# Kernel optimization log

Measured on AMD Instinct MI355X. Metric: run time of the kernel, lower is better.

Reference implementation:

```python
import jax, jax.numpy as jnp
import numpy as np
import math

B, S, H, NH = 1, 2048, 1024, 16  # batch, seq, hidden, heads


def setup_inputs() -> dict:
    key = jax.random.key(0)
    ks = jax.random.split(key, 12)
    inp = {
        "query": jax.random.normal(ks[0], (B, S, H), dtype=jnp.float32),
        "key": jax.random.normal(ks[1], (B, S, H), dtype=jnp.float32),
        "value": jax.random.normal(ks[2], (B, S, H), dtype=jnp.float32),
        "attention_mask": jax.random.randint(ks[3], (1, 1, S, S), 0, 2, dtype=jnp.int32),
        # torch nn.Linear params: y = x @ W.T + b, W init ~ U(-1/sqrt(H), 1/sqrt(H))
        "Wq": jax.random.uniform(ks[4], (H, H), jnp.float32, -1, 1) / math.sqrt(H),
        "bq": jax.random.uniform(ks[5], (H,), jnp.float32, -1, 1) / math.sqrt(H),
        "Wk": jax.random.uniform(ks[6], (H, H), jnp.float32, -1, 1) / math.sqrt(H),
        "bk": jax.random.uniform(ks[7], (H,), jnp.float32, -1, 1) / math.sqrt(H),
        "Wv": jax.random.uniform(ks[8], (H, H), jnp.float32, -1, 1) / math.sqrt(H),
        "bv": jax.random.uniform(ks[9], (H,), jnp.float32, -1, 1) / math.sqrt(H),
        "Wo": jax.random.uniform(ks[10], (H, H), jnp.float32, -1, 1) / math.sqrt(H),
        "bo": jax.random.uniform(ks[11], (H,), jnp.float32, -1, 1) / math.sqrt(H),
        "head": NH,
        "hidden_size": H,
    }
    return inp


def reference(query, key, value, attention_mask, Wq, bq, Wk, bk, Wv, bv, Wo, bo, head, hidden_size):
    b, s, _ = query.shape
    d_k = hidden_size // head

    def proj(x, W, bias):
        # [b, s, hidden] -> [b, head, s, d_k]
        y = x @ W.T + bias
        return y.reshape(b, s, head, d_k).transpose(0, 2, 1, 3)

    q = proj(query, Wq, bq)
    k = proj(key, Wk, bk)
    v = proj(value, Wv, bv)

    # naive full score matrix, as in the source (scale by sqrt(d_k) = last dim of q)
    scores = jnp.einsum("bhqd,bhkd->bhqk", q, k) / math.sqrt(d_k)
    # faithful quirk: masked positions are set to 0 (not -inf) before softmax
    scores = jnp.where(attention_mask == 0, jnp.zeros((), scores.dtype), scores)
    attn = jax.nn.softmax(scores, axis=-1)

    out = jnp.einsum("bhqk,bhkd->bhqd", attn, v)  # [b, head, s, d_k]
    out = out.transpose(0, 2, 1, 3).reshape(b, s, head * d_k)
    return out @ Wo.T + bo
```

## Files before the change

### kernel.cpp

```cpp
#include <hip/hip_runtime.h>
#include <hip/hip_bf16.h>


#define S_LEN 2048
#define HID   1024
#define NHEAD 16
#define DK    64

typedef unsigned short u16;
typedef __attribute__((ext_vector_type(8))) short bf16x8;
typedef __attribute__((ext_vector_type(4))) short bf16x4;
typedef __attribute__((ext_vector_type(4))) float f32x4;

__device__ __forceinline__ void load16_lds(const void* g, void* l) {
  __builtin_amdgcn_global_load_lds(
      (const __attribute__((address_space(1))) void*)g,
      (__attribute__((address_space(3))) void*)l, 16, 0, 0);
}

__device__ __forceinline__ short bfbits(float x) {
  __hip_bfloat16 h = __float2bfloat16(x);
  return *(short*)&h;
}
__device__ __forceinline__ bf16x8 cvt8(float4 a, float4 b) {
  bf16x8 r;
  r[0] = bfbits(a.x); r[1] = bfbits(a.y); r[2] = bfbits(a.z); r[3] = bfbits(a.w);
  r[4] = bfbits(b.x); r[5] = bfbits(b.y); r[6] = bfbits(b.z); r[7] = bfbits(b.w);
  return r;
}
__device__ __forceinline__ float bf2f(u16 u) {
  unsigned v = (unsigned)u << 16;
  return *(float*)&v;
}

__global__ __launch_bounds__(256) void cvtW_kernel(
    const float* __restrict__ wq, const float* __restrict__ wk,
    const float* __restrict__ wv, const float* __restrict__ wo,
    u16* __restrict__ Wbf) {
  const int y = blockIdx.y;
  const float* src = y == 0 ? wq : (y == 1 ? wk : (y == 2 ? wv : wo));
  size_t i = ((size_t)blockIdx.x * 256 + threadIdx.x) * 8;
  float4 a = *(const float4*)(src + i);
  float4 b = *(const float4*)(src + i + 4);
  *(bf16x8*)(Wbf + (size_t)y * (HID * HID) + i) = cvt8(a, b);
}

__global__ void pack_mask_kernel(const int* __restrict__ mask,
                                 unsigned int* __restrict__ bits) {
  int w = blockIdx.x * blockDim.x + threadIdx.x;
  const int4* p = (const int4*)(mask + (size_t)w * 32);
  unsigned word = 0;
#pragma unroll
  for (int i = 0; i < 8; ++i) {
    int4 v = p[i];
    word |= (unsigned)(v.x != 0) << (i * 4 + 0);
    word |= (unsigned)(v.y != 0) << (i * 4 + 1);
    word |= (unsigned)(v.z != 0) << (i * 4 + 2);
    word |= (unsigned)(v.w != 0) << (i * 4 + 3);
  }
  bits[w] = word;
}

__global__ __launch_bounds__(256) void gemm_bt(
    const void* A0, const void* A1, const void* A2, int a_fp32,
    const u16* __restrict__ Wbase,
    const float* b0, const float* b1, const float* b2,
    void* C0, void* C1, void* C2,
    int store_fp32, int transpose_z2, int qscale_z0) {
  constexpr int Mm = 2048, Nn = 1024, Kk = 1024;
  const int z = blockIdx.z;
  const void* A    = z == 0 ? A0 : (z == 1 ? A1 : A2);
  const u16*  W    = Wbase + (size_t)z * (Nn * Kk);
  const float* bias = z == 0 ? b0 : (z == 1 ? b1 : b2);
  void*       C    = z == 0 ? C0 : (z == 1 ? C1 : C2);
  const int transpose = (z == 2) ? transpose_z2 : 0;
  const float oscale = (z == 0 && qscale_z0) ? 0.125f : 1.0f;

  const int tid  = threadIdx.x;
  const int lane = tid & 63, wave = tid >> 6;
  const int q4 = lane >> 4, c16 = lane & 15;
  const int mBase = blockIdx.y * 128, nBase = blockIdx.x * 128;
  const int wm = (wave >> 1) * 64, wn = (wave & 1) * 64;

  __shared__ __align__(16) u16 As[128 * 32];
  __shared__ __align__(16) u16 Bs[128 * 32];

  f32x4 acc[4][4] = {};

  const int srow = lane >> 2;
  const int skk  = (lane & 3) * 8;

  const u16*   Ab = (const u16*)A;
  const float* Af = (const float*)A;

  for (int k0 = 0; k0 < Kk; k0 += 32) {
    float4 apre[4];
    if (a_fp32) {
#pragma unroll
      for (int i = 0; i < 2; ++i) {
        const float* s = Af + (size_t)(mBase + (wave * 2 + i) * 16 + srow) * Kk +
                         k0 + skk;
        apre[2 * i]     = *(const float4*)s;
        apre[2 * i + 1] = *(const float4*)(s + 4);
      }
    }
    __syncthreads();
    if (a_fp32) {
#pragma unroll
      for (int i = 0; i < 2; ++i) {
        int ch = wave * 2 + i;
        *(bf16x8*)&As[ch * 512 + srow * 32 + skk] =
            cvt8(apre[2 * i], apre[2 * i + 1]);
      }
    } else {
#pragma unroll
      for (int i = 0; i < 2; ++i) {
        int ch = wave * 2 + i;
        load16_lds(Ab + (size_t)(mBase + ch * 16 + srow) * Kk + k0 + skk,
                   &As[ch * 512]);
      }
    }
#pragma unroll
    for (int i = 0; i < 2; ++i) {
      int ch = wave * 2 + i;
      load16_lds(W + (size_t)(nBase + ch * 16 + srow) * Kk + k0 + skk,
                 &Bs[ch * 512]);
    }
    __syncthreads();

    bf16x8 af[4], bfr[4];
#pragma unroll
    for (int t = 0; t < 4; ++t) {
      af[t]  = *(const bf16x8*)&As[(wm + t * 16 + c16) * 32 + q4 * 8];
      bfr[t] = *(const bf16x8*)&Bs[(wn + t * 16 + c16) * 32 + q4 * 8];
    }
#pragma unroll
    for (int mt = 0; mt < 4; ++mt)
#pragma unroll
      for (int nt = 0; nt < 4; ++nt)
        acc[mt][nt] = __builtin_amdgcn_mfma_f32_16x16x32_bf16(
            af[mt], bfr[nt], acc[mt][nt], 0, 0, 0);
  }

#pragma unroll
  for (int nt = 0; nt < 4; ++nt) {
    int col = nBase + wn + nt * 16 + c16;
    float bv = bias[col];
#pragma unroll
    for (int mt = 0; mt < 4; ++mt) {
#pragma unroll
      for (int r = 0; r < 4; ++r) {
        int row = mBase + wm + mt * 16 + q4 * 4 + r;
        float v = (acc[mt][nt][r] + bv) * oscale;
        if (store_fp32)
          ((float*)C)[(size_t)row * Nn + col] = v;
        else if (transpose)
          ((__hip_bfloat16*)C)[(size_t)col * Mm + row] = __float2bfloat16(v);
        else
          ((__hip_bfloat16*)C)[(size_t)row * Nn + col] = __float2bfloat16(v);
      }
    }
  }
}

__global__ __launch_bounds__(256) void attn_kernel(
    const u16* __restrict__ Qb, const u16* __restrict__ Kb,
    const u16* __restrict__ Vt, const unsigned* __restrict__ mbits,
    u16* __restrict__ partO, float* __restrict__ partL) {
  const int qt = blockIdx.x;
  const int h  = blockIdx.y;
  const int zz = blockIdx.z;
  const int tid  = threadIdx.x;
  const int lane = tid & 63, wave = tid >> 6;
  const int q4 = lane >> 4, c16 = lane & 15;

  __shared__ __align__(16) u16 Ks[2][64 * 32];
  __shared__ __align__(16) u16 Vs[2][64 * 32];
  __shared__ __align__(16) u16 Ps[4][2 * 16 * 72];

  const int wq0 = qt * 128 + wave * 32;

  bf16x8 qf[2][2];
#pragma unroll
  for (int t = 0; t < 2; ++t)
#pragma unroll
    for (int kk = 0; kk < 2; ++kk)
      qf[t][kk] = *(const bf16x8*)(Qb + (size_t)(wq0 + t * 16 + c16) * HID +
                                   h * DK + kk * 32 + q4 * 8);

  f32x4 o[2][4] = {};
  float l_lane[2][4] = {};

  const int srow = lane >> 2;
  const int se8  = (lane & 3) * 8;
  const int kvbase = zz * (S_LEN / 2);

  for (int it = 0; it < S_LEN / 2 / 64; ++it) {
    const int kv0 = kvbase + it * 64;
    __syncthreads();
#pragma unroll
    for (int j = 0; j < 2; ++j) {
      int ch = wave * 2 + j;
      int half = ch >> 2, grp = ch & 3;
      load16_lds(Kb + (size_t)(kv0 + grp * 16 + srow) * HID + h * DK +
                     half * 32 + se8,
                 &Ks[half][grp * 512]);
      load16_lds(Vt + (size_t)(h * DK + grp * 16 + srow) * S_LEN + kv0 +
                     half * 32 + se8,
                 &Vs[half][grp * 512]);
    }
    __syncthreads();

    f32x4 sv[2][4];
#pragma unroll
    for (int nt = 0; nt < 4; ++nt) {
      bf16x8 kf0 = *(const bf16x8*)&Ks[0][(nt * 16 + c16) * 32 + q4 * 8];
      bf16x8 kf1 = *(const bf16x8*)&Ks[1][(nt * 16 + c16) * 32 + q4 * 8];
#pragma unroll
      for (int t = 0; t < 2; ++t) {
        f32x4 a = {};
        a = __builtin_amdgcn_mfma_f32_16x16x32_bf16(qf[t][0], kf0, a, 0, 0, 0);
        a = __builtin_amdgcn_mfma_f32_16x16x32_bf16(qf[t][1], kf1, a, 0, 0, 0);
        sv[t][nt] = a;
      }
    }

#pragma unroll
    for (int t = 0; t < 2; ++t)
#pragma unroll
      for (int r = 0; r < 4; ++r) {
        int row = wq0 + t * 16 + q4 * 4 + r;
        const unsigned* mrow = mbits + (size_t)row * 64 + (kv0 >> 5);
        unsigned w0 = mrow[0], w1 = mrow[1];
#pragma unroll
        for (int nt = 0; nt < 4; ++nt) {
          unsigned word = (nt < 2) ? w0 : w1;
          int bit = ((nt & 1) * 16) + c16;
          float s = ((word >> bit) & 1u) ? sv[t][nt][r] : 0.0f;
          float p = __expf(s);
          sv[t][nt][r] = p;
          l_lane[t][r] += p;
        }
      }

    u16* pw = &Ps[wave][0];
#pragma unroll
    for (int t = 0; t < 2; ++t)
#pragma unroll
      for (int r = 0; r < 4; ++r)
#pragma unroll
        for (int nt = 0; nt < 4; ++nt)
          ((__hip_bfloat16*)pw)[t * 1152 + (q4 * 4 + r) * 72 + nt * 16 + c16] =
              __float2bfloat16(sv[t][nt][r]);
    asm volatile("s_waitcnt lgkmcnt(0)" ::: "memory");

    bf16x8 vb[2][4];
#pragma unroll
    for (int kk = 0; kk < 2; ++kk)
#pragma unroll
      for (int nt = 0; nt < 4; ++nt)
        vb[kk][nt] = *(const bf16x8*)&Vs[kk][(nt * 16 + c16) * 32 + q4 * 8];
#pragma unroll
    for (int t = 0; t < 2; ++t)
#pragma unroll
      for (int kk = 0; kk < 2; ++kk) {
        bf16x8 pa = *(const bf16x8*)&pw[t * 1152 + c16 * 72 + kk * 32 + q4 * 8];
#pragma unroll
        for (int nt = 0; nt < 4; ++nt)
          o[t][nt] = __builtin_amdgcn_mfma_f32_16x16x32_bf16(pa, vb[kk][nt],
                                                             o[t][nt], 0, 0, 0);
      }
  }

#pragma unroll
  for (int t = 0; t < 2; ++t)
#pragma unroll
    for (int r = 0; r < 4; ++r) {
      float s = l_lane[t][r];
#pragma unroll
      for (int d = 1; d < 16; d <<= 1) s += __shfl_xor(s, d);
      l_lane[t][r] = s;
    }

#pragma unroll
  for (int t = 0; t < 2; ++t)
#pragma unroll
    for (int r = 0; r < 4; ++r) {
      int row = wq0 + t * 16 + q4 * 4 + r;
#pragma unroll
      for (int nt = 0; nt < 4; ++nt)
        ((__hip_bfloat16*)partO)[((size_t)zz * S_LEN + row) * HID + h * DK +
                                 nt * 16 + c16] = __float2bfloat16(o[t][nt][r]);
      if (c16 == 0)
        partL[((size_t)zz * NHEAD + h) * S_LEN + row] = l_lane[t][r];
    }
}

__global__ __launch_bounds__(256) void combine_kernel(
    const u16* __restrict__ partO, const float* __restrict__ partL,
    u16* __restrict__ ctx) {
  size_t idx = ((size_t)blockIdx.x * 256 + threadIdx.x) * 4;
  int row = (int)(idx >> 10);
  int col = (int)(idx & 1023);
  int h = col >> 6;
  float l = partL[(size_t)h * S_LEN + row] +
            partL[((size_t)NHEAD + h) * S_LEN + row];
  float inv = 1.0f / l;
  bf16x4 a = *(const bf16x4*)(partO + idx);
  bf16x4 b = *(const bf16x4*)(partO + (size_t)S_LEN * HID + idx);
  bf16x4 r;
#pragma unroll
  for (int j = 0; j < 4; ++j) {
    float v = (bf2f((u16)a[j]) + bf2f((u16)b[j])) * inv;
    r[j] = bfbits(v);
  }
  *(bf16x4*)(ctx + idx) = r;
}

extern "C" void kernel_launch(void* const* d_in, const int* in_sizes, int n_in,
                              void* d_out, int out_size, void* d_ws, size_t ws_size,
                              hipStream_t stream) {
  const float* q    = (const float*)d_in[0];
  const float* k    = (const float*)d_in[1];
  const float* v    = (const float*)d_in[2];
  const int*   mask = (const int*)d_in[3];
  const float* Wq = (const float*)d_in[4];
  const float* bq = (const float*)d_in[5];
  const float* Wk = (const float*)d_in[6];
  const float* bk = (const float*)d_in[7];
  const float* Wv = (const float*)d_in[8];
  const float* bv = (const float*)d_in[9];
  const float* Wo = (const float*)d_in[10];
  const float* bo = (const float*)d_in[11];

  const size_t M2 = (size_t)S_LEN * HID;
  const size_t need = (4 + 2 + 2 + 2 + 2) * M2 * 2 +
                      (size_t)S_LEN * 64 * 4 + 2 * NHEAD * S_LEN * 4;
  if (ws_size < need) return;

  u16* Wbf   = (u16*)d_ws;
  u16* partO = Wbf + 4 * (size_t)HID * HID / 2 * 2;
  u16* Qb    = partO + 2 * M2;
  u16* Kb    = Qb + M2;
  u16* Vt    = Kb + M2;
  unsigned* mbits = (unsigned*)(Vt + M2);
  float* partL = (float*)(mbits + (size_t)S_LEN * 64);
  u16* ctx = Qb;

  hipLaunchKernelGGL(cvtW_kernel, dim3(512, 4), dim3(256), 0, stream,
                     Wq, Wk, Wv, Wo, Wbf);

  hipLaunchKernelGGL(pack_mask_kernel, dim3((S_LEN * (S_LEN / 32)) / 256),
                     dim3(256), 0, stream, mask, mbits);

  hipLaunchKernelGGL(gemm_bt, dim3(HID / 128, S_LEN / 128, 3), dim3(256), 0,
                     stream, q, k, v, 1, Wbf, bq, bk, bv,
                     Qb, Kb, Vt, 0, 1, 1);

  hipLaunchKernelGGL(attn_kernel, dim3(S_LEN / 128, NHEAD, 2), dim3(256), 0,
                     stream, Qb, Kb, Vt, mbits, partO, partL);

  hipLaunchKernelGGL(combine_kernel, dim3((S_LEN * HID / 4) / 256), dim3(256),
                     0, stream, partO, partL, ctx);

  hipLaunchKernelGGL(gemm_bt, dim3(HID / 128, S_LEN / 128, 1), dim3(256), 0,
                     stream, ctx, ctx, ctx, 0, Wbf + 3 * (size_t)HID * HID,
                     bo, bo, bo, d_out, d_out, d_out, 1, 0, 0);
}
```

Before: 231.0 us.

## Double-buffer GEMM and attention LDS loads, template GEMM tile sizes

```diff
diff --git a/kernel.cpp b/kernel.cpp
--- a/kernel.cpp
+++ b/kernel.cpp
@@ -61,13 +61,20 @@
   bits[w] = word;
 }
 
+template <int BM, bool ABF>
 __global__ __launch_bounds__(256) void gemm_bt(
-    const void* A0, const void* A1, const void* A2, int a_fp32,
+    const void* A0, const void* A1, const void* A2,
     const u16* __restrict__ Wbase,
     const float* b0, const float* b1, const float* b2,
     void* C0, void* C1, void* C2,
     int store_fp32, int transpose_z2, int qscale_z0) {
-  constexpr int Mm = 2048, Nn = 1024, Kk = 1024;
+  constexpr int Mm = 2048, Nn = 1024, Kk = 1024, BK = 64;
+  constexpr int NIT = Kk / BK;
+  constexpr int MT = BM / 32;
+  constexpr int MTILES = Mm / BM;
+  constexpr int AG = BM / 16;
+  constexpr int AU = 2 * AG / 4;
+
   const int z = blockIdx.z;
   const void* A    = z == 0 ? A0 : (z == 1 ? A1 : A2);
   const u16*  W    = Wbase + (size_t)z * (Nn * Kk);
@@ -76,70 +83,100 @@
   const int transpose = (z == 2) ? transpose_z2 : 0;
   const float oscale = (z == 0 && qscale_z0) ? 0.125f : 1.0f;
 
-  const int tid  = threadIdx.x;
-  const int lane = tid & 63, wave = tid >> 6;
+  const int tid = threadIdx.x, lane = tid & 63, wave = tid >> 6;
   const int q4 = lane >> 4, c16 = lane & 15;
-  const int mBase = blockIdx.y * 128, nBase = blockIdx.x * 128;
-  const int wm = (wave >> 1) * 64, wn = (wave & 1) * 64;
-
-  __shared__ __align__(16) u16 As[128 * 32];
-  __shared__ __align__(16) u16 Bs[128 * 32];
-
-  f32x4 acc[4][4] = {};
+  const int bLin = blockIdx.x + blockIdx.y * gridDim.x;
+  const int mBase = (bLin & (MTILES - 1)) * BM;
+  const int nBase = (bLin / MTILES) * 128;
+  const int wm = (wave >> 1) * (BM / 2), wn = (wave & 1) * 64;
+
+  __shared__ __align__(16) u16 As[2][2][BM * 32];
+  __shared__ __align__(16) u16 Bs[2][2][128 * 32];
+
+  f32x4 acc[MT][4] = {};
 
   const int srow = lane >> 2;
-  const int skk  = (lane & 3) * 8;
+  const int se8  = (lane & 3) * 8;
 
   const u16*   Ab = (const u16*)A;
   const float* Af = (const float*)A;
 
-  for (int k0 = 0; k0 < Kk; k0 += 32) {
-    float4 apre[4];
-    if (a_fp32) {
-#pragma unroll
-      for (int i = 0; i < 2; ++i) {
-        const float* s = Af + (size_t)(mBase + (wave * 2 + i) * 16 + srow) * Kk +
-                         k0 + skk;
-        apre[2 * i]     = *(const float4*)s;
-        apre[2 * i + 1] = *(const float4*)(s + 4);
-      }
-    }
+  auto issueW = [&](int it, int buf) {
+#pragma unroll
+    for (int j = 0; j < 4; ++j) {
+      int i = wave * 4 + j;
+      int h = i >> 3, grp = i & 7;
+      load16_lds(W + (size_t)(nBase + grp * 16 + srow) * Kk + it * BK +
+                     h * 32 + se8,
+                 &Bs[buf][h][grp * 512]);
+    }
+  };
+  auto issueA = [&](int it, int buf) {
+#pragma unroll
+    for (int j = 0; j < AU; ++j) {
+      int i = wave * AU + j;
+      int h = i / AG, grp = i % AG;
+      load16_lds(Ab + (size_t)(mBase + grp * 16 + srow) * Kk + it * BK +
+                     h * 32 + se8,
+                 &As[buf][h][grp * 512]);
+    }
+  };
+  float4 ar[AU][2];
+  auto loadA = [&](int it) {
+#pragma unroll
+    for (int j = 0; j < AU; ++j) {
+      int i = wave * AU + j;
+      int h = i / AG, grp = i % AG;
+      const float* s = Af + (size_t)(mBase + grp * 16 + srow) * Kk + it * BK +
+                       h * 32 + se8;
+      ar[j][0] = *(const float4*)s;
+      ar[j][1] = *(const float4*)(s + 4);
+    }
+  };
+  auto storeA = [&](int buf) {
+#pragma unroll
+    for (int j = 0; j < AU; ++j) {
+      int i = wave * AU + j;
+      int h = i / AG, grp = i % AG;
+      *(bf16x8*)&As[buf][h][grp * 512 + srow * 32 + se8] =
+          cvt8(ar[j][0], ar[j][1]);
+    }
+  };
+
+  issueW(0, 0);
+  if (ABF) {
+    issueA(0, 0);
+  } else {
+    loadA(0);
+    storeA(0);
+  }
+  __syncthreads();
+
+  for (int it = 0; it < NIT; ++it) {
+    const int buf = it & 1, nbuf = buf ^ 1;
+    if (it + 1 < NIT) {
+      issueW(it + 1, nbuf);
+      if (ABF) issueA(it + 1, nbuf);
+      else     loadA(it + 1);
+    }
+#pragma unroll
+    for (int kk = 0; kk < 2; ++kk) {
+      bf16x8 af[MT], bfr[4];
+#pragma unroll
+      for (int t = 0; t < MT; ++t)
+        af[t] = *(const bf16x8*)&As[buf][kk][(wm + t * 16 + c16) * 32 + q4 * 8];
+#pragma unroll
+      for (int t = 0; t < 4; ++t)
+        bfr[t] = *(const bf16x8*)&Bs[buf][kk][(wn + t * 16 + c16) * 32 + q4 * 8];
+#pragma unroll
+      for (int mt = 0; mt < MT; ++mt)
+#pragma unroll
+        for (int nt = 0; nt < 4; ++nt)
+          acc[mt][nt] = __builtin_amdgcn_mfma_f32_16x16x32_bf16(
+              af[mt], bfr[nt], acc[mt][nt], 0, 0, 0);
+    }
+    if (!ABF && it + 1 < NIT) storeA(nbuf);
     __syncthreads();
-    if (a_fp32) {
-#pragma unroll
-      for (int i = 0; i < 2; ++i) {
-        int ch = wave * 2 + i;
-        *(bf16x8*)&As[ch * 512 + srow * 32 + skk] =
-            cvt8(apre[2 * i], apre[2 * i + 1]);
-      }
-    } else {
-#pragma unroll
-      for (int i = 0; i < 2; ++i) {
-        int ch = wave * 2 + i;
-        load16_lds(Ab + (size_t)(mBase + ch * 16 + srow) * Kk + k0 + skk,
-                   &As[ch * 512]);
-      }
-    }
-#pragma unroll
-    for (int i = 0; i < 2; ++i) {
-      int ch = wave * 2 + i;
-      load16_lds(W + (size_t)(nBase + ch * 16 + srow) * Kk + k0 + skk,
-                 &Bs[ch * 512]);
-    }
-    __syncthreads();
-
-    bf16x8 af[4], bfr[4];
-#pragma unroll
-    for (int t = 0; t < 4; ++t) {
-      af[t]  = *(const bf16x8*)&As[(wm + t * 16 + c16) * 32 + q4 * 8];
-      bfr[t] = *(const bf16x8*)&Bs[(wn + t * 16 + c16) * 32 + q4 * 8];
-    }
-#pragma unroll
-    for (int mt = 0; mt < 4; ++mt)
-#pragma unroll
-      for (int nt = 0; nt < 4; ++nt)
-        acc[mt][nt] = __builtin_amdgcn_mfma_f32_16x16x32_bf16(
-            af[mt], bfr[nt], acc[mt][nt], 0, 0, 0);
   }
 
 #pragma unroll
@@ -147,7 +184,7 @@
     int col = nBase + wn + nt * 16 + c16;
     float bv = bias[col];
 #pragma unroll
-    for (int mt = 0; mt < 4; ++mt) {
+    for (int mt = 0; mt < MT; ++mt) {
 #pragma unroll
       for (int r = 0; r < 4; ++r) {
         int row = mBase + wm + mt * 16 + q4 * 4 + r;
@@ -167,15 +204,13 @@
     const u16* __restrict__ Qb, const u16* __restrict__ Kb,
     const u16* __restrict__ Vt, const unsigned* __restrict__ mbits,
     u16* __restrict__ partO, float* __restrict__ partL) {
-  const int qt = blockIdx.x;
-  const int h  = blockIdx.y;
-  const int zz = blockIdx.z;
-  const int tid  = threadIdx.x;
-  const int lane = tid & 63, wave = tid >> 6;
+  constexpr int NITA = S_LEN / 2 / 64;
+  const int qt = blockIdx.x, h = blockIdx.y, zz = blockIdx.z;
+  const int tid = threadIdx.x, lane = tid & 63, wave = tid >> 6;
   const int q4 = lane >> 4, c16 = lane & 15;
 
-  __shared__ __align__(16) u16 Ks[2][64 * 32];
-  __shared__ __align__(16) u16 Vs[2][64 * 32];
+  __shared__ __align__(16) u16 Ks[2][2][64 * 32];
+  __shared__ __align__(16) u16 Vs[2][2][64 * 32];
   __shared__ __align__(16) u16 Ps[4][2 * 16 * 72];
 
   const int wq0 = qt * 128 + wave * 32;
@@ -195,27 +230,34 @@
   const int se8  = (lane & 3) * 8;
   const int kvbase = zz * (S_LEN / 2);
 
-  for (int it = 0; it < S_LEN / 2 / 64; ++it) {
+  auto issueKV = [&](int it, int buf) {
     const int kv0 = kvbase + it * 64;
-    __syncthreads();
 #pragma unroll
     for (int j = 0; j < 2; ++j) {
       int ch = wave * 2 + j;
       int half = ch >> 2, grp = ch & 3;
       load16_lds(Kb + (size_t)(kv0 + grp * 16 + srow) * HID + h * DK +
                      half * 32 + se8,
-                 &Ks[half][grp * 512]);
+                 &Ks[buf][half][grp * 512]);
       load16_lds(Vt + (size_t)(h * DK + grp * 16 + srow) * S_LEN + kv0 +
                      half * 32 + se8,
-                 &Vs[half][grp * 512]);
-    }
-    __syncthreads();
+                 &Vs[buf][half][grp * 512]);
+    }
+  };
+
+  issueKV(0, 0);
+  __syncthreads();
+
+  for (int it = 0; it < NITA; ++it) {
+    const int buf = it & 1, nbuf = buf ^ 1;
+    const int kv0 = kvbase + it * 64;
+    if (it + 1 < NITA) issueKV(it + 1, nbuf);
 
     f32x4 sv[2][4];
 #pragma unroll
     for (int nt = 0; nt < 4; ++nt) {
-      bf16x8 kf0 = *(const bf16x8*)&Ks[0][(nt * 16 + c16) * 32 + q4 * 8];
-      bf16x8 kf1 = *(const bf16x8*)&Ks[1][(nt * 16 + c16) * 32 + q4 * 8];
+      bf16x8 kf0 = *(const bf16x8*)&Ks[buf][0][(nt * 16 + c16) * 32 + q4 * 8];
+      bf16x8 kf1 = *(const bf16x8*)&Ks[buf][1][(nt * 16 + c16) * 32 + q4 * 8];
 #pragma unroll
       for (int t = 0; t < 2; ++t) {
         f32x4 a = {};
@@ -259,7 +301,8 @@
     for (int kk = 0; kk < 2; ++kk)
 #pragma unroll
       for (int nt = 0; nt < 4; ++nt)
-        vb[kk][nt] = *(const bf16x8*)&Vs[kk][(nt * 16 + c16) * 32 + q4 * 8];
+        vb[kk][nt] =
+            *(const bf16x8*)&Vs[buf][kk][(nt * 16 + c16) * 32 + q4 * 8];
 #pragma unroll
     for (int t = 0; t < 2; ++t)
 #pragma unroll
@@ -270,6 +313,7 @@
           o[t][nt] = __builtin_amdgcn_mfma_f32_16x16x32_bf16(pa, vb[kk][nt],
                                                              o[t][nt], 0, 0, 0);
       }
+    __syncthreads();
   }
 
 #pragma unroll
@@ -353,9 +397,9 @@
   hipLaunchKernelGGL(pack_mask_kernel, dim3((S_LEN * (S_LEN / 32)) / 256),
                      dim3(256), 0, stream, mask, mbits);
 
-  hipLaunchKernelGGL(gemm_bt, dim3(HID / 128, S_LEN / 128, 3), dim3(256), 0,
-                     stream, q, k, v, 1, Wbf, bq, bk, bv,
-                     Qb, Kb, Vt, 0, 1, 1);
+  hipLaunchKernelGGL((gemm_bt<128, false>), dim3(8, 16, 3), dim3(256), 0,
+                     stream, q, k, v, Wbf, bq, bk, bv,
+                     (void*)Qb, (void*)Kb, (void*)Vt, 0, 1, 1);
 
   hipLaunchKernelGGL(attn_kernel, dim3(S_LEN / 128, NHEAD, 2), dim3(256), 0,
                      stream, Qb, Kb, Vt, mbits, partO, partL);
@@ -363,7 +407,7 @@
   hipLaunchKernelGGL(combine_kernel, dim3((S_LEN * HID / 4) / 256), dim3(256),
                      0, stream, partO, partL, ctx);
 
-  hipLaunchKernelGGL(gemm_bt, dim3(HID / 128, S_LEN / 128, 1), dim3(256), 0,
-                     stream, ctx, ctx, ctx, 0, Wbf + 3 * (size_t)HID * HID,
+  hipLaunchKernelGGL((gemm_bt<64, true>), dim3(8, 32, 1), dim3(256), 0,
+                     stream, ctx, ctx, ctx, Wbf + 3 * (size_t)HID * HID,
                      bo, bo, bo, d_out, d_out, d_out, 1, 0, 0);
 }
```

Measured after the change: 222.8 us. 3.5% less time.
